# Optimization experiments

Hardware: AMD Instinct MI355X
Metric: run time of the kernel (lower is better)

Reference implementation:

```python
import jax, jax.numpy as jnp
import numpy as np

N = 50000      # nodes
E = 800000     # directed edges (before self loops)
B = 64         # graphs in batch
F_IN = 128     # input_dim
POS = 16       # pos_dim
H = 4          # heads
C = 64         # hidden_dim (per head)
HC = H * C     # 256
OUT = 128      # output_dim
ENH = F_IN + POS
EPS = 1e-5
NEG_SLOPE = 0.2


def setup_inputs() -> dict:
    key = jax.random.key(0)
    ks = jax.random.split(key, 20)
    s = 0.05
    inp = {
        "x": jax.random.normal(ks[0], (N, F_IN), jnp.float32),
        "edge_index": jax.random.randint(ks[1], (2, E), 0, N, jnp.int32),
        "batch": (jnp.arange(N, dtype=jnp.int32) // ((N + B - 1) // B)).astype(jnp.int32),
        "W_pos": jax.random.normal(ks[2], (2, POS), jnp.float32) * s,
        "b_pos": jnp.zeros((POS,), jnp.float32),
        "W1": jax.random.normal(ks[3], (ENH, HC), jnp.float32) * s,
        "a_src1": jax.random.normal(ks[4], (H, C), jnp.float32) * s,
        "a_dst1": jax.random.normal(ks[5], (H, C), jnp.float32) * s,
        "b1": jnp.zeros((HC,), jnp.float32),
        "gamma1": jnp.ones((HC,), jnp.float32),
        "beta1": jnp.zeros((HC,), jnp.float32),
        "W2": jax.random.normal(ks[6], (HC, HC), jnp.float32) * s,
        "a_src2": jax.random.normal(ks[7], (H, C), jnp.float32) * s,
        "a_dst2": jax.random.normal(ks[8], (H, C), jnp.float32) * s,
        "b2": jnp.zeros((HC,), jnp.float32),
        "gamma2": jnp.ones((HC,), jnp.float32),
        "beta2": jnp.zeros((HC,), jnp.float32),
        "W_fc": jax.random.normal(ks[9], (HC, OUT), jnp.float32) * s,
        "b_fc": jnp.zeros((OUT,), jnp.float32),
    }
    return inp


def _positions(batch):
    # vectorized equivalent of _generate_positions (grid layout per graph)
    ones = jnp.ones((N,), jnp.float32)
    counts = jax.ops.segment_sum(ones, batch, num_segments=B)          # [B]
    starts = jnp.cumsum(counts) - counts                               # [B]
    i = jnp.arange(N, dtype=jnp.float32) - starts[batch]               # index within graph
    gs = jnp.ceil(jnp.sqrt(counts)).astype(jnp.int32)                  # grid size per graph
    g = gs[batch]
    ii = i.astype(jnp.int32)
    row = ii // g
    col = ii % g
    denom = jnp.maximum(g - 1, 1).astype(jnp.float32)
    return jnp.stack([row.astype(jnp.float32) / denom,
                      col.astype(jnp.float32) / denom], axis=1)        # [N, 2]


def _gat(x, W, a_src, a_dst, bias, src, dst):
    # PyG GATConv (concat heads, add_self_loops already in src/dst)
    h = (x @ W).reshape(N, H, C)                                       # [N,H,C]
    alpha_s = jnp.sum(h * a_src, axis=-1)                              # [N,H]
    alpha_d = jnp.sum(h * a_dst, axis=-1)                              # [N,H]
    e = jax.nn.leaky_relu(alpha_s[src] + alpha_d[dst], NEG_SLOPE)      # [Etot,H]
    e_max = jax.ops.segment_max(e, dst, num_segments=N)                # [N,H]
    e_max = jax.lax.stop_gradient(jnp.where(jnp.isfinite(e_max), e_max, 0.0))
    ex = jnp.exp(e - e_max[dst])
    denom = jax.ops.segment_sum(ex, dst, num_segments=N)               # [N,H]
    alpha = ex / denom[dst]                                            # softmax over incoming edges
    msg = h[src] * alpha[:, :, None]                                   # [Etot,H,C]
    out = jax.ops.segment_sum(msg, dst, num_segments=N)                # [N,H,C]
    return out.reshape(N, HC) + bias


def _bn(x, gamma, beta):
    m = jnp.mean(x, axis=0)
    v = jnp.var(x, axis=0)
    return gamma * (x - m) * jax.lax.rsqrt(v + EPS) + beta


def reference(x, edge_index, batch, W_pos, b_pos,
              W1, a_src1, a_dst1, b1, gamma1, beta1,
              W2, a_src2, a_dst2, b2, gamma2, beta2,
              W_fc, b_fc):
    pos = _positions(batch)
    pe = pos @ W_pos + b_pos                                           # [N,POS]
    h = jnp.concatenate([x, pe], axis=1)                               # [N,ENH]
    loops = jnp.arange(N, dtype=edge_index.dtype)
    src = jnp.concatenate([edge_index[0], loops])
    dst = jnp.concatenate([edge_index[1], loops])
    h = jax.nn.elu(_bn(_gat(h, W1, a_src1, a_dst1, b1, src, dst), gamma1, beta1))
    h = jax.nn.elu(_bn(_gat(h, W2, a_src2, a_dst2, b2, src, dst), gamma2, beta2))
    # global mean pool per graph
    counts = jax.ops.segment_sum(jnp.ones((N,), h.dtype), batch, num_segments=B)
    pooled = jax.ops.segment_sum(h, batch, num_segments=B) / counts[:, None]
    return pooled @ W_fc + b_fc                                        # [B,OUT]
```

## Files before the change

kernel.cpp:

```cpp
#include <hip/hip_runtime.h>
#include <math.h>

#define POSD 16
#define DEG_CAP 64
#define NSLICE 16
#define AGG_BLOCKS 2048

typedef __attribute__((ext_vector_type(8))) __bf16 bf16x8;
typedef __attribute__((ext_vector_type(4))) float f32x4;

__device__ __forceinline__ unsigned short f2bf(float f){
  unsigned int u = __float_as_uint(f);
  u += 0x7FFF + ((u >> 16) & 1);
  return (unsigned short)(u >> 16);
}
__device__ __forceinline__ float bf2f(unsigned short u){
  return __uint_as_float(((unsigned int)u) << 16);
}

__global__ __launch_bounds__(256) void k_init(
    const int* __restrict__ batch, int* __restrict__ starts,
    const int* __restrict__ src, const int* __restrict__ dst,
    int* __restrict__ cnt, int* __restrict__ csr_src,
    float* __restrict__ bnP,
    const float* __restrict__ W_pos, const float* __restrict__ b_pos,
    const float* __restrict__ W1, const float* __restrict__ W2,
    unsigned short* __restrict__ W1t, unsigned short* __restrict__ W2t,
    float* __restrict__ uvw,
    int N, int E, int nfb){
  int bx = blockIdx.x;
  int t = threadIdx.x;
  if (bx < nfb){
    int i = bx * 256 + t;
    if (i < 2 * NSLICE * 512) bnP[i] = 0.f;
    if (i < N){
      int bi = batch[i];
      int bp = (i == 0) ? -1 : batch[i - 1];
      for (int b = bp + 1; b <= bi; ++b) starts[b] = i;
      if (i == N - 1){
        for (int b = bi + 1; b <= 64; ++b) starts[b] = N;
      }
    }
    if (i < E){
      int d = dst[i];
      int slot = atomicAdd(&cnt[d], 1);
      csr_src[(size_t)d * DEG_CAP + slot] = src[i];
    }
  } else if (bx < nfb + 128){
    int idx = (bx - nfb) * 256 + t;
    int n = idx >> 7, k = idx & 127;
    W1t[idx] = f2bf(W1[(size_t)k * 256 + n]);
  } else if (bx < nfb + 128 + 256){
    int j = (bx - nfb - 128) * 256 + t;
    int n = j >> 8, k = j & 255;
    W2t[j] = f2bf(W2[(size_t)k * 256 + n]);
  } else {
    float u = 0.f, v = 0.f, wv = 0.f;
    #pragma unroll
    for (int k = 0; k < POSD; ++k){
      float wc = W1[(size_t)(128 + k) * 256 + t];
      u  += W_pos[k] * wc;
      v  += W_pos[POSD + k] * wc;
      wv += b_pos[k] * wc;
    }
    uvw[t] = u; uvw[256 + t] = v; uvw[512 + t] = wv;
  }
}

#define LDST 40
template<int MODE>
__global__ __launch_bounds__(256) void k_mfma_gemm(
    const unsigned short* __restrict__ A, const float* __restrict__ Af,
    const unsigned short* __restrict__ Bt,
    unsigned short* __restrict__ C,
    const float* __restrict__ a_src, const float* __restrict__ a_dst,
    float* __restrict__ alpS, float* __restrict__ alpD, int M, int Kp,
    const float* __restrict__ uvw, const int* __restrict__ batch,
    const int* __restrict__ starts,
    const float* __restrict__ bnP, const float* __restrict__ gamma,
    const float* __restrict__ beta, float invN){
  __shared__ unsigned short As[128 * LDST];
  __shared__ unsigned short Bs[128 * LDST];
  __shared__ float bn_sc[256];
  __shared__ float bn_sh[256];
  int t = threadIdx.x;
  int lane = t & 63, wave = t >> 6;
  int wm = (wave >> 1) * 64, wn = (wave & 1) * 64;
  int quad = lane >> 4, l16 = lane & 15;
  int row0 = blockIdx.x * 128;
  int n0 = blockIdx.y * 128;

  if (MODE == 1){
    float s = 0.f, q = 0.f;
    #pragma unroll
    for (int j = 0; j < NSLICE; ++j){
      s += bnP[j * 512 + t];
      q += bnP[j * 512 + 256 + t];
    }
    float mean = s * invN;
    float var = q * invN - mean * mean;
    float inv = rsqrtf(var + 1e-5f);
    float g = gamma[t];
    bn_sc[t] = g * inv;
    bn_sh[t] = beta[t] - mean * g * inv;
    __syncthreads();
  }

  f32x4 acc[4][4] = {};

  int eA0 = t, eA1 = t + 256;
  for (int kk = 0; kk < Kp; kk += 32){
    #pragma unroll
    for (int rep = 0; rep < 2; ++rep){
      int e = rep ? eA1 : eA0;
      int r = e >> 2, s = e & 3;
      int grow = row0 + r;
      if (MODE == 0){
        float4 f0 = make_float4(0.f, 0.f, 0.f, 0.f), f1 = f0;
        if (grow < M){
          const float4* xs = (const float4*)(Af + (size_t)grow * Kp + kk + s * 8);
          f0 = xs[0]; f1 = xs[1];
        }
        ushort4 o0, o1;
        o0.x = f2bf(f0.x); o0.y = f2bf(f0.y); o0.z = f2bf(f0.z); o0.w = f2bf(f0.w);
        o1.x = f2bf(f1.x); o1.y = f2bf(f1.y); o1.z = f2bf(f1.z); o1.w = f2bf(f1.w);
        *(ushort4*)&As[r * LDST + s * 8] = o0;
        *(ushort4*)&As[r * LDST + s * 8 + 4] = o1;
      } else {
        uint4 va = make_uint4(0, 0, 0, 0);
        if (grow < M) va = *(const uint4*)(A + (size_t)grow * Kp + kk + s * 8);
        unsigned int* wvp = (unsigned int*)&va;
        int cbase = kk + s * 8;
        #pragma unroll
        for (int h = 0; h < 4; ++h){
          unsigned int res = 0;
          #pragma unroll
          for (int kb = 0; kb < 2; ++kb){
            int cc = cbase + h * 2 + kb;
            float xv = bf2f((unsigned short)((wvp[h] >> (16 * kb)) & 0xFFFF));
            float y = bn_sc[cc] * xv + bn_sh[cc];
            y = (y > 0.f) ? y : (__expf(y) - 1.f);
            res |= ((unsigned int)f2bf(y)) << (16 * kb);
          }
          wvp[h] = res;
        }
        *(uint4*)&As[r * LDST + s * 8] = va;
      }
      uint4 vb = *(const uint4*)(Bt + (size_t)(n0 + r) * Kp + kk + s * 8);
      *(uint4*)&Bs[r * LDST + s * 8] = vb;
    }
    __syncthreads();
    bf16x8 af[4], bfr[4];
    #pragma unroll
    for (int i = 0; i < 4; ++i)
      af[i] = *(const bf16x8*)&As[(wm + i * 16 + l16) * LDST + quad * 8];
    #pragma unroll
    for (int j = 0; j < 4; ++j)
      bfr[j] = *(const bf16x8*)&Bs[(wn + j * 16 + l16) * LDST + quad * 8];
    #pragma unroll
    for (int i = 0; i < 4; ++i)
      #pragma unroll
      for (int j = 0; j < 4; ++j)
        acc[i][j] = __builtin_amdgcn_mfma_f32_16x16x32_bf16(af[i], bfr[j], acc[i][j], 0, 0, 0);
    __syncthreads();
  }

  if (MODE == 0){
    float uu[4], vv[4], ww[4];
    #pragma unroll
    for (int j = 0; j < 4; ++j){
      int col = n0 + wn + j * 16 + l16;
      uu[j] = uvw[col]; vv[j] = uvw[256 + col]; ww[j] = uvw[512 + col];
    }
    #pragma unroll
    for (int i = 0; i < 4; ++i){
      #pragma unroll
      for (int r = 0; r < 4; ++r){
        int row = row0 + wm + i * 16 + quad * 4 + r;
        if (row < M){
          int b = batch[row];
          int st = starts[b];
          int cc = starts[b + 1] - st;
          int g2 = (int)ceilf(sqrtf((float)cc));
          int dd = g2 - 1; if (dd < 1) dd = 1;
          float idn = 1.0f / (float)dd;
          int ii = row - st;
          int irow = ii / g2;
          int icol = ii - irow * g2;
          float rn = (float)irow * idn, cn = (float)icol * idn;
          #pragma unroll
          for (int j = 0; j < 4; ++j)
            acc[i][j][r] += rn * uu[j] + cn * vv[j] + ww[j];
        }
      }
    }
  }

  #pragma unroll
  for (int i = 0; i < 4; ++i){
    int rbase = row0 + wm + i * 16 + quad * 4;
    #pragma unroll
    for (int j = 0; j < 4; ++j){
      int col = n0 + wn + j * 16 + l16;
      #pragma unroll
      for (int r = 0; r < 4; ++r){
        int row = rbase + r;
        if (row < M) C[(size_t)row * 256 + col] = f2bf(acc[i][j][r]);
      }
    }
  }
  int hda = (n0 + wn) >> 6;
  float asw[4], adw[4];
  #pragma unroll
  for (int j = 0; j < 4; ++j){
    int c = n0 + wn + j * 16 + l16;
    asw[j] = a_src[c];
    adw[j] = a_dst[c];
  }
  #pragma unroll
  for (int i = 0; i < 4; ++i){
    #pragma unroll
    for (int r = 0; r < 4; ++r){
      int row = row0 + wm + i * 16 + quad * 4 + r;
      float ps = acc[i][0][r] * asw[0] + acc[i][1][r] * asw[1]
               + acc[i][2][r] * asw[2] + acc[i][3][r] * asw[3];
      float pd = acc[i][0][r] * adw[0] + acc[i][1][r] * adw[1]
               + acc[i][2][r] * adw[2] + acc[i][3][r] * adw[3];
      ps += __shfl_xor(ps, 1); ps += __shfl_xor(ps, 2);
      ps += __shfl_xor(ps, 4); ps += __shfl_xor(ps, 8);
      pd += __shfl_xor(pd, 1); pd += __shfl_xor(pd, 2);
      pd += __shfl_xor(pd, 4); pd += __shfl_xor(pd, 8);
      if (l16 == 0 && row < M){
        alpS[row * 4 + hda] = ps;
        alpD[row * 4 + hda] = pd;
      }
    }
  }
}

__global__ __launch_bounds__(256) void k_aggregate(const unsigned short* __restrict__ hlin,
                                                   const float* __restrict__ alpS,
                                                   const float* __restrict__ alpD,
                                                   const int* __restrict__ cnt,
                                                   const int* __restrict__ csr_src,
                                                   const float* __restrict__ bias,
                                                   unsigned short* __restrict__ outb,
                                                   float* __restrict__ bnP,
                                                   int N, int ngroups){
  __shared__ float rs[4][256];
  __shared__ float rq[4][256];
  int wv = threadIdx.x >> 6;
  int lane = threadIdx.x & 63;
  int hd = lane >> 4;
  int hd2 = lane & 3;
  int eloc = lane >> 2;
  const unsigned short* hbase = hlin + (size_t)lane * 4;
  float4 bv = *(const float4*)(bias + lane * 4);

  float s0 = 0.f, s1 = 0.f, s2 = 0.f, s3 = 0.f;
  float q0 = 0.f, q1 = 0.f, q2 = 0.f, q3 = 0.f;

  for (int grp = blockIdx.x; grp < ngroups; grp += gridDim.x){
    int n = grp * 4 + wv;
    if (n < N){
      int beg = n << 6;
      int deg = cnt[n];
      int total = deg + 1;
      float ad2 = alpD[n * 4 + hd2];
      float lsum = 0.f;
      float a0 = 0.f, a1 = 0.f, a2 = 0.f, a3 = 0.f;

      int full = total & ~15;
      for (int base = 0; base < full; base += 16){
        int e = base + eloc;
        int s = (e < deg) ? csr_src[beg + e] : n;
        float xv = alpS[s * 4 + hd2] + ad2;
        float sc = (xv >= 0.f) ? xv : 0.2f * xv;
        float p = __expf(sc);
        lsum += p;
        uint2 v[16];
        #pragma unroll
        for (int j2 = 0; j2 < 16; ++j2){
          int sj = __shfl(s, j2 << 2);
          v[j2] = *(const uint2*)(hbase + (size_t)sj * 256);
        }
        #pragma unroll
        for (int j2 = 0; j2 < 16; ++j2){
          float pj = __shfl(p, (j2 << 2) | hd);
          a0 += pj * __uint_as_float(v[j2].x << 16);
          a1 += pj * __uint_as_float(v[j2].x & 0xFFFF0000u);
          a2 += pj * __uint_as_float(v[j2].y << 16);
          a3 += pj * __uint_as_float(v[j2].y & 0xFFFF0000u);
        }
      }
      int rem = total - full;
      if (rem){
        int e = full + eloc;
        int s = n;
        float p = 0.f;
        if (eloc < rem){
          if (e < deg) s = csr_src[beg + e];
          float xv = alpS[s * 4 + hd2] + ad2;
          float sc = (xv >= 0.f) ? xv : 0.2f * xv;
          p = __expf(sc);
        }
        lsum += p;
        #pragma unroll
        for (int g = 0; g < 4; ++g){
          if (g * 4 < rem){
            uint2 v[4];
            #pragma unroll
            for (int q = 0; q < 4; ++q){
              int j2 = g * 4 + q;
              int sj = __shfl(s, j2 << 2);
              v[q] = *(const uint2*)(hbase + (size_t)sj * 256);
            }
            #pragma unroll
            for (int q = 0; q < 4; ++q){
              int j2 = g * 4 + q;
              float pj = __shfl(p, (j2 << 2) | hd);
              a0 += pj * __uint_as_float(v[q].x << 16);
              a1 += pj * __uint_as_float(v[q].x & 0xFFFF0000u);
              a2 += pj * __uint_as_float(v[q].y << 16);
              a3 += pj * __uint_as_float(v[q].y & 0xFFFF0000u);
            }
          }
        }
      }
      lsum += __shfl_xor(lsum, 4);
      lsum += __shfl_xor(lsum, 8);
      lsum += __shfl_xor(lsum, 16);
      lsum += __shfl_xor(lsum, 32);
      float lh = __shfl(lsum, hd);
      float inv = 1.0f / lh;
      ushort4 o;
      o.x = f2bf(a0 * inv + bv.x);
      o.y = f2bf(a1 * inv + bv.y);
      o.z = f2bf(a2 * inv + bv.z);
      o.w = f2bf(a3 * inv + bv.w);
      *(ushort4*)(outb + (size_t)n * 256 + lane * 4) = o;
      float f0 = bf2f(o.x), f1 = bf2f(o.y), f2 = bf2f(o.z), f3 = bf2f(o.w);
      s0 += f0; s1 += f1; s2 += f2; s3 += f3;
      q0 += f0 * f0; q1 += f1 * f1; q2 += f2 * f2; q3 += f3 * f3;
    }
  }

  int c0 = lane * 4;
  rs[wv][c0 + 0] = s0; rs[wv][c0 + 1] = s1;
  rs[wv][c0 + 2] = s2; rs[wv][c0 + 3] = s3;
  rq[wv][c0 + 0] = q0; rq[wv][c0 + 1] = q1;
  rq[wv][c0 + 2] = q2; rq[wv][c0 + 3] = q3;
  __syncthreads();
  int t = threadIdx.x;
  float s = rs[0][t] + rs[1][t] + rs[2][t] + rs[3][t];
  float q = rq[0][t] + rq[1][t] + rq[2][t] + rq[3][t];
  float* bp = bnP + (size_t)(blockIdx.x & (NSLICE - 1)) * 512;
  atomicAdd(&bp[t], s);
  atomicAdd(&bp[256 + t], q);
}

__global__ __launch_bounds__(1024) void k_tail(
    const unsigned short* __restrict__ in, const float* __restrict__ bnP,
    const float* __restrict__ gamma, const float* __restrict__ beta,
    const int* __restrict__ starts, const float* __restrict__ W_fc,
    const float* __restrict__ b_fc, float* __restrict__ out, float invN){
  __shared__ float pm[4][256];
  __shared__ float scs[256], shs[256];
  int t = threadIdx.x;
  int c = t & 255;
  int seg = t >> 8;
  if (t < 256){
    float s = 0.f, q = 0.f;
    #pragma unroll
    for (int j = 0; j < NSLICE; ++j){
      s += bnP[j * 512 + t];
      q += bnP[j * 512 + 256 + t];
    }
    float mean = s * invN;
    float var = q * invN - mean * mean;
    float inv = rsqrtf(var + 1e-5f);
    float g = gamma[t];
    scs[t] = g * inv;
    shs[t] = beta[t] - mean * g * inv;
  }
  __syncthreads();
  int b = blockIdx.x;
  int r0 = starts[b], r1 = starts[b + 1];
  float scl = scs[c], shf = shs[c];
  float acc = 0.f;
  #pragma unroll 4
  for (int r = r0 + seg; r < r1; r += 4){
    float y = scl * bf2f(in[(size_t)r * 256 + c]) + shf;
    y = (y > 0.f) ? y : (__expf(y) - 1.f);
    acc += y;
  }
  pm[seg][c] = acc;
  __syncthreads();
  if (t < 256){
    int cnt = r1 - r0;
    float ic = (cnt > 0) ? 1.0f / (float)cnt : 0.f;
    pm[0][t] = (pm[0][t] + pm[1][t] + pm[2][t] + pm[3][t]) * ic;
  }
  __syncthreads();
  if (t < 128){
    float a = b_fc[t];
    #pragma unroll 4
    for (int cc = 0; cc < 256; ++cc) a += pm[0][cc] * W_fc[cc * 128 + t];
    out[b * 128 + t] = a;
  }
}

extern "C" void kernel_launch(void* const* d_in, const int* in_sizes, int n_in,
                              void* d_out, int out_size, void* d_ws, size_t ws_size,
                              hipStream_t stream){
  const float* x      = (const float*)d_in[0];
  const int*   eidx   = (const int*)  d_in[1];
  const int*   batch  = (const int*)  d_in[2];
  const float* W_pos  = (const float*)d_in[3];
  const float* b_pos  = (const float*)d_in[4];
  const float* W1     = (const float*)d_in[5];
  const float* a_src1 = (const float*)d_in[6];
  const float* a_dst1 = (const float*)d_in[7];
  const float* b1     = (const float*)d_in[8];
  const float* gamma1 = (const float*)d_in[9];
  const float* beta1  = (const float*)d_in[10];
  const float* W2     = (const float*)d_in[11];
  const float* a_src2 = (const float*)d_in[12];
  const float* a_dst2 = (const float*)d_in[13];
  const float* b2     = (const float*)d_in[14];
  const float* gamma2 = (const float*)d_in[15];
  const float* beta2  = (const float*)d_in[16];
  const float* W_fc   = (const float*)d_in[17];
  const float* b_fc   = (const float*)d_in[18];
  float* out = (float*)d_out;

  const int N = in_sizes[0] / 128;
  const int E = in_sizes[1] / 2;
  const int* esrc = eidx;
  const int* edst = eidx + E;

  char* w = (char*)d_ws;
  size_t off = 0;
  auto alloc = [&](size_t bytes) -> void* {
    void* p = w + off;
    off = (off + bytes + 255) & ~(size_t)255;
    return p;
  };
  unsigned short* X1b  = (unsigned short*)alloc((size_t)N * 256 * 2);
  unsigned short* A1b  = (unsigned short*)alloc((size_t)N * 256 * 2);
  float* alpS    = (float*)alloc((size_t)N * 4 * 4);
  float* alpD    = (float*)alloc((size_t)N * 4 * 4);
  int*   starts  = (int*)  alloc(65 * 4);
  int*   cnt     = (int*)  alloc((size_t)N * 4);
  int*   csr_src = (int*)  alloc((size_t)N * DEG_CAP * 4);
  float* bnP     = (float*)alloc((size_t)2 * NSLICE * 512 * 4);
  unsigned short* W1t = (unsigned short*)alloc(256 * 128 * 2);
  unsigned short* W2t = (unsigned short*)alloc(256 * 256 * 2);
  float* uvw = (float*)alloc(3 * 256 * 4);
  float* bnP1 = bnP, *bnP2 = bnP + NSLICE * 512;

  hipMemsetAsync(cnt, 0, (size_t)N * 4, stream);

  const int nfb = (E + 255) / 256;
  const int ngroups = (N + 3) / 4;

  k_init<<<nfb + 128 + 256 + 1, 256, 0, stream>>>(
      batch, starts, esrc, edst, cnt, csr_src, bnP,
      W_pos, b_pos, W1, W2, W1t, W2t, uvw, N, E, nfb);

  dim3 ggrid((N + 127) / 128, 2);
  const float invN = 1.0f / (float)N;

  k_mfma_gemm<0><<<ggrid, 256, 0, stream>>>(nullptr, x, W1t, X1b, a_src1, a_dst1,
                                            alpS, alpD, N, 128, uvw, batch, starts,
                                            nullptr, nullptr, nullptr, 0.f);
  k_aggregate<<<AGG_BLOCKS, 256, 0, stream>>>(X1b, alpS, alpD, cnt, csr_src, b1,
                                              A1b, bnP1, N, ngroups);

  k_mfma_gemm<1><<<ggrid, 256, 0, stream>>>(A1b, nullptr, W2t, X1b, a_src2, a_dst2,
                                            alpS, alpD, N, 256, nullptr, nullptr, nullptr,
                                            bnP1, gamma1, beta1, invN);
  k_aggregate<<<AGG_BLOCKS, 256, 0, stream>>>(X1b, alpS, alpD, cnt, csr_src, b2,
                                              A1b, bnP2, N, ngroups);

  k_tail<<<64, 1024, 0, stream>>>(A1b, bnP2, gamma2, beta2, starts, W_fc, b_fc,
                                  out, invN);
}
```

Baseline: 398.2 us.

## Split tail pooling across four blocks per graph and coarsen init edge loop

The tail kernel now launches four blocks per graph. Each block pools a strided quarter of the rows and accumulates into a global pooled buffer with atomics. A per-graph completion counter lets the last block finish the mean and the final FC layer. Separately, the init kernel's edge/CSR section now handles four elements per thread, with a quarter as many blocks. This adds parallelism to the 64-block tail at the cost of extra atomics and a last-block handshake.

```diff
diff --git a/kernel.cpp b/kernel.cpp
--- a/kernel.cpp
+++ b/kernel.cpp
@@ -22,7 +22,7 @@
     const int* __restrict__ batch, int* __restrict__ starts,
     const int* __restrict__ src, const int* __restrict__ dst,
     int* __restrict__ cnt, int* __restrict__ csr_src,
-    float* __restrict__ bnP,
+    float* __restrict__ bnP, float* __restrict__ pooled, int* __restrict__ dcnt,
     const float* __restrict__ W_pos, const float* __restrict__ b_pos,
     const float* __restrict__ W1, const float* __restrict__ W2,
     unsigned short* __restrict__ W1t, unsigned short* __restrict__ W2t,
@@ -31,20 +31,26 @@
   int bx = blockIdx.x;
   int t = threadIdx.x;
   if (bx < nfb){
-    int i = bx * 256 + t;
-    if (i < 2 * NSLICE * 512) bnP[i] = 0.f;
-    if (i < N){
-      int bi = batch[i];
-      int bp = (i == 0) ? -1 : batch[i - 1];
-      for (int b = bp + 1; b <= bi; ++b) starts[b] = i;
-      if (i == N - 1){
-        for (int b = bi + 1; b <= 64; ++b) starts[b] = N;
-      }
-    }
-    if (i < E){
-      int d = dst[i];
-      int slot = atomicAdd(&cnt[d], 1);
-      csr_src[(size_t)d * DEG_CAP + slot] = src[i];
+    int base = bx * 1024 + t;
+    #pragma unroll
+    for (int u = 0; u < 4; ++u){
+      int i = base + u * 256;
+      if (i < 2 * NSLICE * 512) bnP[i] = 0.f;
+      if (i < 64 * 256) pooled[i] = 0.f;
+      if (i < 64) dcnt[i] = 0;
+      if (i < N){
+        int bi = batch[i];
+        int bp = (i == 0) ? -1 : batch[i - 1];
+        for (int b = bp + 1; b <= bi; ++b) starts[b] = i;
+        if (i == N - 1){
+          for (int b = bi + 1; b <= 64; ++b) starts[b] = N;
+        }
+      }
+      if (i < E){
+        int d = dst[i];
+        int slot = atomicAdd(&cnt[d], 1);
+        csr_src[(size_t)d * DEG_CAP + slot] = src[i];
+      }
     }
   } else if (bx < nfb + 128){
     int idx = (bx - nfb) * 256 + t;
@@ -363,9 +369,11 @@
     const unsigned short* __restrict__ in, const float* __restrict__ bnP,
     const float* __restrict__ gamma, const float* __restrict__ beta,
     const int* __restrict__ starts, const float* __restrict__ W_fc,
-    const float* __restrict__ b_fc, float* __restrict__ out, float invN){
+    const float* __restrict__ b_fc, float* __restrict__ out,
+    float* __restrict__ pooled, int* __restrict__ dcnt, float invN){
   __shared__ float pm[4][256];
   __shared__ float scs[256], shs[256];
+  __shared__ int lastf;
   int t = threadIdx.x;
   int c = t & 255;
   int seg = t >> 8;
@@ -384,12 +392,12 @@
     shs[t] = beta[t] - mean * g * inv;
   }
   __syncthreads();
-  int b = blockIdx.x;
+  int b = blockIdx.x >> 2;
+  int q4 = blockIdx.x & 3;
   int r0 = starts[b], r1 = starts[b + 1];
   float scl = scs[c], shf = shs[c];
   float acc = 0.f;
-  #pragma unroll 4
-  for (int r = r0 + seg; r < r1; r += 4){
+  for (int r = r0 + q4 * 4 + seg; r < r1; r += 16){
     float y = scl * bf2f(in[(size_t)r * 256 + c]) + shf;
     y = (y > 0.f) ? y : (__expf(y) - 1.f);
     acc += y;
@@ -397,16 +405,29 @@
   pm[seg][c] = acc;
   __syncthreads();
   if (t < 256){
-    int cnt = r1 - r0;
-    float ic = (cnt > 0) ? 1.0f / (float)cnt : 0.f;
-    pm[0][t] = (pm[0][t] + pm[1][t] + pm[2][t] + pm[3][t]) * ic;
+    float s = pm[0][t] + pm[1][t] + pm[2][t] + pm[3][t];
+    atomicAdd(&pooled[b * 256 + t], s);
   }
   __syncthreads();
-  if (t < 128){
-    float a = b_fc[t];
-    #pragma unroll 4
-    for (int cc = 0; cc < 256; ++cc) a += pm[0][cc] * W_fc[cc * 128 + t];
-    out[b * 128 + t] = a;
+  if (t == 0){
+    int old = atomicAdd(&dcnt[b], 1);
+    lastf = (old == 3);
+  }
+  __syncthreads();
+  if (lastf){
+    if (t < 256){
+      float tot = atomicAdd(&pooled[b * 256 + t], 0.f);
+      int cntn = r1 - r0;
+      float ic = (cntn > 0) ? 1.0f / (float)cntn : 0.f;
+      pm[0][t] = tot * ic;
+    }
+    __syncthreads();
+    if (t < 128){
+      float a = b_fc[t];
+      #pragma unroll 4
+      for (int cc = 0; cc < 256; ++cc) a += pm[0][cc] * W_fc[cc * 128 + t];
+      out[b * 128 + t] = a;
+    }
   }
 }
 
@@ -454,6 +475,8 @@
   int*   cnt     = (int*)  alloc((size_t)N * 4);
   int*   csr_src = (int*)  alloc((size_t)N * DEG_CAP * 4);
   float* bnP     = (float*)alloc((size_t)2 * NSLICE * 512 * 4);
+  float* pooled  = (float*)alloc(64 * 256 * 4);
+  int*   dcnt    = (int*)  alloc(64 * 4);
   unsigned short* W1t = (unsigned short*)alloc(256 * 128 * 2);
   unsigned short* W2t = (unsigned short*)alloc(256 * 256 * 2);
   float* uvw = (float*)alloc(3 * 256 * 4);
@@ -461,11 +484,11 @@
 
   hipMemsetAsync(cnt, 0, (size_t)N * 4, stream);
 
-  const int nfb = (E + 255) / 256;
+  const int nfb = (E + 1023) / 1024;
   const int ngroups = (N + 3) / 4;
 
   k_init<<<nfb + 128 + 256 + 1, 256, 0, stream>>>(
-      batch, starts, esrc, edst, cnt, csr_src, bnP,
+      batch, starts, esrc, edst, cnt, csr_src, bnP, pooled, dcnt,
       W_pos, b_pos, W1, W2, W1t, W2t, uvw, N, E, nfb);
 
   dim3 ggrid((N + 127) / 128, 2);
@@ -483,6 +506,6 @@
   k_aggregate<<<AGG_BLOCKS, 256, 0, stream>>>(X1b, alpS, alpD, cnt, csr_src, b2,
                                               A1b, bnP2, N, ngroups);
 
-  k_tail<<<64, 1024, 0, stream>>>(A1b, bnP2, gamma2, beta2, starts, W_fc, b_fc,
-                                  out, invN);
-}
+  k_tail<<<256, 1024, 0, stream>>>(A1b, bnP2, gamma2, beta2, starts, W_fc, b_fc,
+                                   out, pooled, dcnt, invN);
+}
```

Measured after the change: 409.4 us. 2.8% more time.
